# Kernel optimization log

Hardware: AMD Instinct MI355X
Metric: run time of the kernel (lower is better)

Reference implementation:

```python
import jax, jax.numpy as jnp
import numpy as np

EMBED_DIM = 1024
NUM_HEADS = 16
HEAD_DIM = EMBED_DIM // NUM_HEADS
B, T = 2, 2048


def setup_inputs() -> dict:
    key = jax.random.key(0)
    ks = jax.random.split(key, 9)
    s = 1.0 / np.sqrt(EMBED_DIM)
    return {
        "x": jax.random.normal(ks[0], (B, T, EMBED_DIM), dtype=jnp.float32),
        "W_q": jax.random.uniform(ks[1], (EMBED_DIM, EMBED_DIM), jnp.float32, -s, s),
        "b_q": jax.random.uniform(ks[2], (EMBED_DIM,), jnp.float32, -s, s),
        "W_k": jax.random.uniform(ks[3], (EMBED_DIM, EMBED_DIM), jnp.float32, -s, s),
        "b_k": jax.random.uniform(ks[4], (EMBED_DIM,), jnp.float32, -s, s),
        "W_v": jax.random.uniform(ks[5], (EMBED_DIM, EMBED_DIM), jnp.float32, -s, s),
        "b_v": jax.random.uniform(ks[6], (EMBED_DIM,), jnp.float32, -s, s),
        "W_o": jax.random.uniform(ks[7], (EMBED_DIM, EMBED_DIM), jnp.float32, -s, s),
        "b_o": jax.random.uniform(ks[8], (EMBED_DIM,), jnp.float32, -s, s),
    }


def reference(x, W_q, b_q, W_k, b_k, W_v, b_v, W_o, b_o):
    Bv, Tv, C = x.shape
    # QKV projections (torch Linear: x @ W.T + b); split into heads -> (B,H,T,Dh)
    def proj(W, b):
        return (x @ W.T + b).reshape(Bv, Tv, NUM_HEADS, HEAD_DIM).transpose(0, 2, 1, 3)
    q, k, v = proj(W_q, b_q), proj(W_k, b_k), proj(W_v, b_v)
    scale = 1.0 / np.sqrt(HEAD_DIM).astype(np.float32)
    scores = jnp.einsum("bhqd,bhkd->bhqk", q, k) * scale  # (B,H,T,T)
    causal = jnp.tril(jnp.ones((Tv, Tv), dtype=bool))
    scores = jnp.where(causal, scores, -jnp.inf)
    attn = jax.nn.softmax(scores, axis=-1)
    # dropout is identity in eval / p=0
    out = jnp.einsum("bhqk,bhkd->bhqd", attn, v)  # (B,H,T,Dh)
    out = out.transpose(0, 2, 1, 3).reshape(Bv, Tv, C)
    return out @ W_o.T + b_o
```

## Files before the change

### kernel.cpp

```cpp
#include <hip/hip_runtime.h>
#include <hip/hip_bf16.h>


typedef __bf16 bf16;
typedef __attribute__((ext_vector_type(8))) __bf16 bf16x8;
typedef __attribute__((ext_vector_type(4))) __bf16 bf16x4;
typedef __attribute__((ext_vector_type(4))) float floatx4;
typedef __attribute__((ext_vector_type(4))) short short4v;

#define LOG2E 1.44269504088896340736f

__device__ __forceinline__ void gl2lds16(const void* g, void* l) {
  __builtin_amdgcn_global_load_lds((const __attribute__((address_space(1))) void*)g,
                                   (__attribute__((address_space(3))) void*)l, 16, 0, 0);
}

__device__ __forceinline__ floatx4 mfma16(bf16x4 a, bf16x4 b, floatx4 c) {
#if __has_builtin(__builtin_amdgcn_mfma_f32_16x16x16_bf16)
  return __builtin_amdgcn_mfma_f32_16x16x16_bf16(a, b, c, 0, 0, 0);
#elif __has_builtin(__builtin_amdgcn_mfma_f32_16x16x16bf16_1k)
  return __builtin_amdgcn_mfma_f32_16x16x16bf16_1k(
      __builtin_bit_cast(short4v, a), __builtin_bit_cast(short4v, b), c, 0, 0, 0);
#else
  floatx4 d = c;
  asm volatile("v_mfma_f32_16x16x16_bf16 %0, %1, %2, %0"
               : "+v"(d) : "v"(a), "v"(b));
  return d;
#endif
}

__global__ __launch_bounds__(256) void cast_all(
    const float* __restrict__ x, const float* __restrict__ wq,
    const float* __restrict__ wk, const float* __restrict__ wv,
    const float* __restrict__ wo, bf16* __restrict__ dst)
{
  const size_t M1 = (size_t)1 << 20;
  size_t i4 = ((size_t)blockIdx.x * 256 + threadIdx.x) * 4;
  const float* src = x;
  size_t off = i4;
  if (i4 >= 4 * M1) {
    size_t r = i4 - 4 * M1;
    int seg = (int)(r >> 20);
    off = r & (M1 - 1);
    src = (seg == 0) ? wq : (seg == 1) ? wk : (seg == 2) ? wv : wo;
  }
  float4 f = *(const float4*)(src + off);
  bf16x4 o = { (bf16)f.x, (bf16)f.y, (bf16)f.z, (bf16)f.w };
  *(bf16x4*)(dst + i4) = o;
}

__global__ __launch_bounds__(256, 2) void gemm_qkv(
    const bf16* __restrict__ A, const bf16* __restrict__ Wb,
    const float* __restrict__ bq, const float* __restrict__ bk,
    const float* __restrict__ bv, bf16* __restrict__ Qout,
    bf16* __restrict__ Kout, bf16* __restrict__ vt, float qscale)
{
  constexpr int K = 1024;
  __shared__ bf16 As[128 * 64];
  __shared__ bf16 Bs[3][64 * 64];
  const int tid = threadIdx.x;
  const int lane = tid & 63;
  const int wid = tid >> 6;
  const int l15 = lane & 15, l4 = lane >> 4;
  const int n0 = blockIdx.x << 6;
  const int m0 = blockIdx.y << 7;

  floatx4 acc[3][2][4] = {};

  for (int k0 = 0; k0 < K; k0 += 64) {
#pragma unroll
    for (int it = 0; it < 4; ++it) {
      int c = it * 256 + tid;
      int row = c >> 3, gs = ((c & 7) ^ (row & 7)) << 3;
      gl2lds16(A + (size_t)(m0 + row) * K + k0 + gs, As + c * 8);
    }
#pragma unroll
    for (int mat = 0; mat < 3; ++mat)
#pragma unroll
      for (int it = 0; it < 2; ++it) {
        int c = it * 256 + tid;
        int row = c >> 3, gs = ((c & 7) ^ (row & 7)) << 3;
        gl2lds16(Wb + ((size_t)mat << 20) + (size_t)(n0 + row) * K + k0 + gs,
                 &Bs[mat][c * 8]);
      }
    __syncthreads();
#pragma unroll
    for (int kk = 0; kk < 2; ++kk) {
      bf16x8 af[2];
#pragma unroll
      for (int i = 0; i < 2; ++i) {
        int r = wid * 32 + i * 16 + l15;
        int g = (kk * 4 + l4) ^ (r & 7);
        af[i] = *(const bf16x8*)(As + r * 64 + g * 8);
      }
#pragma unroll
      for (int mat = 0; mat < 3; ++mat) {
        bf16x8 bfr[4];
#pragma unroll
        for (int j = 0; j < 4; ++j) {
          int r = j * 16 + l15;
          int g = (kk * 4 + l4) ^ (r & 7);
          bfr[j] = *(const bf16x8*)(&Bs[mat][r * 64 + g * 8]);
        }
#pragma unroll
        for (int i = 0; i < 2; ++i)
#pragma unroll
          for (int j = 0; j < 4; ++j)
            acc[mat][i][j] = __builtin_amdgcn_mfma_f32_16x16x32_bf16(
                af[i], bfr[j], acc[mat][i][j], 0, 0, 0);
      }
    }
    __syncthreads();
  }

#pragma unroll
  for (int j = 0; j < 4; ++j) {
    int col = n0 + j * 16 + l15;
    float bq_ = bq[col], bk_ = bk[col], bv_ = bv[col];
    int h = col >> 6, d = col & 63;
#pragma unroll
    for (int i = 0; i < 2; ++i) {
      int rbase = m0 + wid * 32 + i * 16 + l4 * 4;
#pragma unroll
      for (int rg = 0; rg < 4; ++rg) {
        int row = rbase + rg;
        Qout[(size_t)row * 1024 + col] = (bf16)((acc[0][i][j][rg] + bq_) * qscale);
        Kout[(size_t)row * 1024 + col] = (bf16)(acc[1][i][j][rg] + bk_);
      }
      int bb = rbase >> 11, t = rbase & 2047;
      int tp = (t & ~31) | (((t >> 2) & 3) << 3) | (((t >> 4) & 1) << 2);
      bf16x4 pk;
#pragma unroll
      for (int rg = 0; rg < 4; ++rg) pk[rg] = (bf16)(acc[2][i][j][rg] + bv_);
      *(bf16x4*)(vt + (((size_t)(bb * 16 + h)) << 17) + ((size_t)d << 11) + tp) = pk;
    }
  }
}

__global__ __launch_bounds__(256, 3) void gemm_out(
    const bf16* __restrict__ A, const bf16* __restrict__ W,
    const float* __restrict__ bias, float* __restrict__ outf, int K, int N)
{
  __shared__ bf16 As[128 * 64];
  __shared__ bf16 Bs[64 * 64];
  const int tid = threadIdx.x;
  const int lane = tid & 63;
  const int wid = tid >> 6;
  const int l15 = lane & 15, l4 = lane >> 4;
  const int n0 = blockIdx.x << 6;
  const int m0 = blockIdx.y << 7;

  floatx4 acc[2][4] = {};

  for (int k0 = 0; k0 < K; k0 += 64) {
#pragma unroll
    for (int it = 0; it < 4; ++it) {
      int c = it * 256 + tid;
      int row = c >> 3, gs = ((c & 7) ^ (row & 7)) << 3;
      gl2lds16(A + (size_t)(m0 + row) * K + k0 + gs, As + c * 8);
    }
#pragma unroll
    for (int it = 0; it < 2; ++it) {
      int c = it * 256 + tid;
      int row = c >> 3, gs = ((c & 7) ^ (row & 7)) << 3;
      gl2lds16(W + (size_t)(n0 + row) * K + k0 + gs, Bs + c * 8);
    }
    __syncthreads();
#pragma unroll
    for (int kk = 0; kk < 2; ++kk) {
      bf16x8 af[2], bfr[4];
#pragma unroll
      for (int i = 0; i < 2; ++i) {
        int r = wid * 32 + i * 16 + l15;
        int g = (kk * 4 + l4) ^ (r & 7);
        af[i] = *(const bf16x8*)(As + r * 64 + g * 8);
      }
#pragma unroll
      for (int j = 0; j < 4; ++j) {
        int r = j * 16 + l15;
        int g = (kk * 4 + l4) ^ (r & 7);
        bfr[j] = *(const bf16x8*)(Bs + r * 64 + g * 8);
      }
#pragma unroll
      for (int i = 0; i < 2; ++i)
#pragma unroll
        for (int j = 0; j < 4; ++j)
          acc[i][j] = __builtin_amdgcn_mfma_f32_16x16x32_bf16(af[i], bfr[j], acc[i][j], 0, 0, 0);
    }
    __syncthreads();
  }

#pragma unroll
  for (int j = 0; j < 4; ++j) {
    int col = n0 + j * 16 + l15;
    float b_ = bias[col];
#pragma unroll
    for (int i = 0; i < 2; ++i)
#pragma unroll
      for (int rg = 0; rg < 4; ++rg) {
        int row = m0 + wid * 32 + i * 16 + l4 * 4 + rg;
        outf[(size_t)row * N + col] = acc[i][j][rg] + b_;
      }
  }
}

__global__ __launch_bounds__(256, 3) void attn_kernel(
    const bf16* __restrict__ Q, const bf16* __restrict__ Kg,
    const bf16* __restrict__ Vt, bf16* __restrict__ AO)
{
  constexpr int T = 2048, C = 1024;
  __shared__ bf16 Ks[2][64 * 64];
  __shared__ bf16 Vts[2][64 * 64];

  const int tid = threadIdx.x;
  const int lane = tid & 63;
  const int w = tid >> 6;
  const int l15 = lane & 15, l4 = lane >> 4;

  const int u = blockIdx.x;
  const int bh = u & 31;
  const int qt = 31 - (u >> 5);
  const int q0 = qt << 6;
  const int nkt = qt + 1;
  const size_t base = ((size_t)(bh >> 4) * T) * C + (bh & 15) * 64;
  const bf16* vtb = Vt + ((size_t)bh << 17);

  auto stageK = [&](int j0, int bufi) {
#pragma unroll
    for (int it = 0; it < 2; ++it) {
      int c = it * 256 + tid;
      int row = c >> 3, g = (c & 7) ^ (row & 7);
      gl2lds16(Kg + base + (size_t)(j0 + row) * C + g * 8, &Ks[bufi][c * 8]);
    }
  };
  auto stageV = [&](int j0, int bufi) {
#pragma unroll
    for (int it = 0; it < 2; ++it) {
      int c = it * 256 + tid;
      int d = c >> 3, g = (c & 7) ^ (d & 7);
      gl2lds16(vtb + ((size_t)d << 11) + j0 + g * 8, &Vts[bufi][c * 8]);
    }
  };

  const int q = q0 + w * 16 + l15;

  bf16x8 qf[2];
  {
    const bf16* qp = Q + base + (size_t)q * C + l4 * 8;
    qf[0] = *(const bf16x8*)(qp);
    qf[1] = *(const bf16x8*)(qp + 32);
  }

  floatx4 o[4] = {};
  float lpart = 0.f;

  stageK(0, 0);
  stageV(0, 0);

  for (int jt = 0; jt < nkt; ++jt) {
    __syncthreads();
    const int cur = jt & 1;
    if (jt + 1 < nkt) {
      stageK((jt + 1) << 6, cur ^ 1);
      stageV((jt + 1) << 6, cur ^ 1);
    }
    const int j0 = jt << 6;

    floatx4 s4[4] = {};
#pragma unroll
    for (int kk = 0; kk < 2; ++kk) {
#pragma unroll
      for (int tj = 0; tj < 4; ++tj) {
        int r = tj * 16 + l15;
        int g = (kk * 4 + l4) ^ (r & 7);
        bf16x8 kf = *(const bf16x8*)(&Ks[cur][r * 64 + g * 8]);
        s4[tj] = __builtin_amdgcn_mfma_f32_16x16x32_bf16(kf, qf[kk], s4[tj], 0, 0, 0);
      }
    }

    if (jt == nkt - 1) {
#pragma unroll
      for (int tj = 0; tj < 4; ++tj) {
        int j = j0 + tj * 16 + l4 * 4;
#pragma unroll
        for (int rg = 0; rg < 4; ++rg)
          if (j + rg > q) s4[tj][rg] = -3e38f;
      }
    }

#pragma unroll
    for (int tj = 0; tj < 4; ++tj)
#pragma unroll
      for (int rg = 0; rg < 4; ++rg) {
        float e = __builtin_amdgcn_exp2f(s4[tj][rg]);
        s4[tj][rg] = e;
        lpart += e;
      }

    bf16x4 pf[4];
#pragma unroll
    for (int tj = 0; tj < 4; ++tj) {
      bf16x4 pk = { (bf16)s4[tj][0], (bf16)s4[tj][1],
                    (bf16)s4[tj][2], (bf16)s4[tj][3] };
      pf[tj] = pk;
    }

#pragma unroll
    for (int tk = 0; tk < 2; ++tk) {
#pragma unroll
      for (int td = 0; td < 4; ++td) {
        int r = td * 16 + l15;
        int g = (tk * 4 + l4) ^ (r & 7);
        bf16x8 vf = *(const bf16x8*)(&Vts[cur][r * 64 + g * 8]);
        bf16x4 lo = { vf[0], vf[1], vf[2], vf[3] };
        bf16x4 hi = { vf[4], vf[5], vf[6], vf[7] };
        o[td] = mfma16(lo, pf[tk * 2], o[td]);
        o[td] = mfma16(hi, pf[tk * 2 + 1], o[td]);
      }
    }
  }

  lpart += __shfl_xor(lpart, 16, 64);
  lpart += __shfl_xor(lpart, 32, 64);
  float inv = 1.0f / lpart;
#pragma unroll
  for (int td = 0; td < 4; ++td) {
    bf16x4 ok = { (bf16)(o[td][0] * inv), (bf16)(o[td][1] * inv),
                  (bf16)(o[td][2] * inv), (bf16)(o[td][3] * inv) };
    *(bf16x4*)(AO + base + (size_t)q * C + td * 16 + l4 * 4) = ok;
  }
}

extern "C" void kernel_launch(void* const* d_in, const int* in_sizes, int n_in,
                              void* d_out, int out_size, void* d_ws, size_t ws_size,
                              hipStream_t stream) {
  const float* x  = (const float*)d_in[0];
  const float* Wq = (const float*)d_in[1];
  const float* bq = (const float*)d_in[2];
  const float* Wk = (const float*)d_in[3];
  const float* bk = (const float*)d_in[4];
  const float* Wv = (const float*)d_in[5];
  const float* bv = (const float*)d_in[6];
  const float* Wo = (const float*)d_in[7];
  const float* bo = (const float*)d_in[8];

  bf16* ws = (bf16*)d_ws;
  const size_t M1 = (size_t)1 << 20;
  bf16* xb  = ws;
  bf16* wqb = ws + 4 * M1;
  bf16* wob = ws + 7 * M1;
  bf16* Qp  = ws + 8 * M1;
  bf16* Kp  = ws + 12 * M1;
  bf16* Vtp = ws + 16 * M1;
  bf16* AOp = ws + 20 * M1;

  cast_all<<<8192, 256, 0, stream>>>(x, Wq, Wk, Wv, Wo, ws);
  gemm_qkv<<<dim3(16, 32), 256, 0, stream>>>(
      xb, wqb, bq, bk, bv, Qp, Kp, Vtp, 0.125f * LOG2E);
  attn_kernel<<<1024, 256, 0, stream>>>(Qp, Kp, Vtp, AOp);
  gemm_out<<<dim3(16, 32), 256, 0, stream>>>(
      AOp, wob, bo, (float*)d_out, 1024, 1024);
}
```

Measured before the change: 169.1 us.

## Restructure QKV GEMM into 256x192 double-buffered tiles with interleaved loads and MFMAs

Rewrites the fused QKV projection GEMM to use 512-thread blocks covering 256x192 output tiles, treating the Q/K/V weights as one concatenated 3072-wide matrix. LDS is double-buffered, and the next tile's global-to-LDS loads are interleaved with MFMA phases using raw s_barrier and s_setprio, in a ping-pong style schedule. A block-index swizzle remaps the 1D grid onto tiles for cache locality. This is meant to hide memory latency and raise operand reuse per block, at the cost of more LDS and registers per block and fewer blocks overall (256).

```diff
diff --git a/kernel.cpp b/kernel.cpp
--- a/kernel.cpp
+++ b/kernel.cpp
@@ -28,6 +28,9 @@
   return d;
 #endif
 }
+
+#define MFMA32 __builtin_amdgcn_mfma_f32_16x16x32_bf16
+#define PBAR asm volatile("s_barrier" ::: "memory")
 
 __global__ __launch_bounds__(256) void cast_all(
     const float* __restrict__ x, const float* __restrict__ wq,
@@ -49,90 +52,164 @@
   *(bf16x4*)(dst + i4) = o;
 }
 
-__global__ __launch_bounds__(256, 2) void gemm_qkv(
+__global__ __launch_bounds__(512, 2) void gemm_qkv(
     const bf16* __restrict__ A, const bf16* __restrict__ Wb,
     const float* __restrict__ bq, const float* __restrict__ bk,
     const float* __restrict__ bv, bf16* __restrict__ Qout,
     bf16* __restrict__ Kout, bf16* __restrict__ vt, float qscale)
 {
   constexpr int K = 1024;
-  __shared__ bf16 As[128 * 64];
-  __shared__ bf16 Bs[3][64 * 64];
+  constexpr int NT = 16;
+  __shared__ bf16 As[2][256 * 64];
+  __shared__ bf16 Bs[2][192 * 64];
+
   const int tid = threadIdx.x;
   const int lane = tid & 63;
   const int wid = tid >> 6;
+  const int wm = wid >> 2;
+  const int wn = wid & 3;
   const int l15 = lane & 15, l4 = lane >> 4;
-  const int n0 = blockIdx.x << 6;
-  const int m0 = blockIdx.y << 7;
-
-  floatx4 acc[3][2][4] = {};
-
-  for (int k0 = 0; k0 < K; k0 += 64) {
+  const int xlo = l15 & 7;
+
+  const int u = blockIdx.x;
+  const int xk = u & 7, s = u >> 3;
+  const int by = xk * 2 + (s & 1);
+  const int bx = s >> 1;
+  const int m0 = by << 8;
+  const int n0 = bx * 192;
+
+  auto stageA = [&](int t) {
+    const int bufi = t & 1;
 #pragma unroll
     for (int it = 0; it < 4; ++it) {
-      int c = it * 256 + tid;
+      int c = it * 512 + tid;
       int row = c >> 3, gs = ((c & 7) ^ (row & 7)) << 3;
-      gl2lds16(A + (size_t)(m0 + row) * K + k0 + gs, As + c * 8);
-    }
-#pragma unroll
-    for (int mat = 0; mat < 3; ++mat)
-#pragma unroll
-      for (int it = 0; it < 2; ++it) {
-        int c = it * 256 + tid;
-        int row = c >> 3, gs = ((c & 7) ^ (row & 7)) << 3;
-        gl2lds16(Wb + ((size_t)mat << 20) + (size_t)(n0 + row) * K + k0 + gs,
-                 &Bs[mat][c * 8]);
-      }
+      gl2lds16(A + (size_t)(m0 + row) * K + t * 64 + gs, &As[bufi][c * 8]);
+    }
+  };
+  auto stageB = [&](int t) {
+    const int bufi = t & 1;
+#pragma unroll
+    for (int it = 0; it < 2; ++it) {
+      int c = it * 512 + tid;
+      int row = c >> 3, gs = ((c & 7) ^ (row & 7)) << 3;
+      gl2lds16(Wb + (size_t)(n0 + row) * K + t * 64 + gs, &Bs[bufi][c * 8]);
+    }
+    {
+      int c = 1024 + tid;
+      int row = c >> 3, gs = ((c & 7) ^ (row & 7)) << 3;
+      gl2lds16(Wb + (size_t)(n0 + row) * K + t * 64 + gs, &Bs[bufi][c * 8]);
+    }
+  };
+
+  floatx4 acc[8][3] = {};
+  bf16x8 a_[4][2];
+  bf16x8 b_[3][2];
+
+  stageA(0);
+  stageB(0);
+  __syncthreads();
+
+  for (int t = 0; t < NT; ++t) {
+    const int cur = t & 1;
+
+#pragma unroll
+    for (int f = 0; f < 4; ++f)
+#pragma unroll
+      for (int kk = 0; kk < 2; ++kk)
+        a_[f][kk] = *(const bf16x8*)(
+            &As[cur][(wm * 128 + f * 16 + l15) * 64 + (((kk * 4 + l4) ^ xlo) << 3)]);
+#pragma unroll
+    for (int j = 0; j < 2; ++j)
+#pragma unroll
+      for (int kk = 0; kk < 2; ++kk)
+        b_[j][kk] = *(const bf16x8*)(
+            &Bs[cur][(wn * 48 + j * 16 + l15) * 64 + (((kk * 4 + l4) ^ xlo) << 3)]);
+    if (t + 1 < NT) stageA(t + 1);
+    PBAR;
+    __builtin_amdgcn_s_setprio(1);
+#pragma unroll
+    for (int f = 0; f < 4; ++f)
+#pragma unroll
+      for (int j = 0; j < 2; ++j)
+#pragma unroll
+        for (int kk = 0; kk < 2; ++kk)
+          acc[f][j] = MFMA32(a_[f][kk], b_[j][kk], acc[f][j], 0, 0, 0);
+    __builtin_amdgcn_s_setprio(0);
+    PBAR;
+
+#pragma unroll
+    for (int kk = 0; kk < 2; ++kk)
+      b_[2][kk] = *(const bf16x8*)(
+          &Bs[cur][(wn * 48 + 32 + l15) * 64 + (((kk * 4 + l4) ^ xlo) << 3)]);
+    if (t + 1 < NT) stageB(t + 1);
+    PBAR;
+    __builtin_amdgcn_s_setprio(1);
+#pragma unroll
+    for (int f = 0; f < 4; ++f)
+#pragma unroll
+      for (int kk = 0; kk < 2; ++kk)
+        acc[f][2] = MFMA32(a_[f][kk], b_[2][kk], acc[f][2], 0, 0, 0);
+    __builtin_amdgcn_s_setprio(0);
+    PBAR;
+
+#pragma unroll
+    for (int f = 0; f < 4; ++f)
+#pragma unroll
+      for (int kk = 0; kk < 2; ++kk)
+        a_[f][kk] = *(const bf16x8*)(
+            &As[cur][(wm * 128 + 64 + f * 16 + l15) * 64 + (((kk * 4 + l4) ^ xlo) << 3)]);
+    PBAR;
+    __builtin_amdgcn_s_setprio(1);
+#pragma unroll
+    for (int f = 0; f < 4; ++f)
+#pragma unroll
+      for (int kk = 0; kk < 2; ++kk)
+        acc[4 + f][2] = MFMA32(a_[f][kk], b_[2][kk], acc[4 + f][2], 0, 0, 0);
+    __builtin_amdgcn_s_setprio(0);
+    PBAR;
+
+    __builtin_amdgcn_s_setprio(1);
+#pragma unroll
+    for (int f = 0; f < 4; ++f)
+#pragma unroll
+      for (int j = 0; j < 2; ++j)
+#pragma unroll
+        for (int kk = 0; kk < 2; ++kk)
+          acc[4 + f][j] = MFMA32(a_[f][kk], b_[j][kk], acc[4 + f][j], 0, 0, 0);
+    __builtin_amdgcn_s_setprio(0);
+
     __syncthreads();
-#pragma unroll
-    for (int kk = 0; kk < 2; ++kk) {
-      bf16x8 af[2];
-#pragma unroll
-      for (int i = 0; i < 2; ++i) {
-        int r = wid * 32 + i * 16 + l15;
-        int g = (kk * 4 + l4) ^ (r & 7);
-        af[i] = *(const bf16x8*)(As + r * 64 + g * 8);
-      }
-#pragma unroll
-      for (int mat = 0; mat < 3; ++mat) {
-        bf16x8 bfr[4];
-#pragma unroll
-        for (int j = 0; j < 4; ++j) {
-          int r = j * 16 + l15;
-          int g = (kk * 4 + l4) ^ (r & 7);
-          bfr[j] = *(const bf16x8*)(&Bs[mat][r * 64 + g * 8]);
-        }
-#pragma unroll
-        for (int i = 0; i < 2; ++i)
-#pragma unroll
-          for (int j = 0; j < 4; ++j)
-            acc[mat][i][j] = __builtin_amdgcn_mfma_f32_16x16x32_bf16(
-                af[i], bfr[j], acc[mat][i][j], 0, 0, 0);
-      }
-    }
-    __syncthreads();
-  }
-
-#pragma unroll
-  for (int j = 0; j < 4; ++j) {
-    int col = n0 + j * 16 + l15;
-    float bq_ = bq[col], bk_ = bk[col], bv_ = bv[col];
-    int h = col >> 6, d = col & 63;
-#pragma unroll
-    for (int i = 0; i < 2; ++i) {
-      int rbase = m0 + wid * 32 + i * 16 + l4 * 4;
-#pragma unroll
-      for (int rg = 0; rg < 4; ++rg) {
-        int row = rbase + rg;
-        Qout[(size_t)row * 1024 + col] = (bf16)((acc[0][i][j][rg] + bq_) * qscale);
-        Kout[(size_t)row * 1024 + col] = (bf16)(acc[1][i][j][rg] + bk_);
-      }
-      int bb = rbase >> 11, t = rbase & 2047;
-      int tp = (t & ~31) | (((t >> 2) & 3) << 3) | (((t >> 4) & 1) << 2);
-      bf16x4 pk;
-#pragma unroll
-      for (int rg = 0; rg < 4; ++rg) pk[rg] = (bf16)(acc[2][i][j][rg] + bv_);
-      *(bf16x4*)(vt + (((size_t)(bb * 16 + h)) << 17) + ((size_t)d << 11) + tp) = pk;
+  }
+
+#pragma unroll
+  for (int f = 0; f < 8; ++f) {
+    int rbase = m0 + wm * 128 + f * 16 + l4 * 4;
+#pragma unroll
+    for (int j = 0; j < 3; ++j) {
+      int col = n0 + wn * 48 + j * 16 + l15;
+      int mat = col >> 10;
+      int c10 = col & 1023;
+      floatx4 v = acc[f][j];
+      if (mat == 0) {
+        float b_ = bq[c10];
+#pragma unroll
+        for (int rg = 0; rg < 4; ++rg)
+          Qout[(size_t)(rbase + rg) * 1024 + c10] = (bf16)((v[rg] + b_) * qscale);
+      } else if (mat == 1) {
+        float b_ = bk[c10];
+#pragma unroll
+        for (int rg = 0; rg < 4; ++rg)
+          Kout[(size_t)(rbase + rg) * 1024 + c10] = (bf16)(v[rg] + b_);
+      } else {
+        float b_ = bv[c10];
+        int h = c10 >> 6, d = c10 & 63;
+        int bb = rbase >> 11, tt = rbase & 2047;
+        int tp = (tt & ~31) | (((tt >> 2) & 3) << 3) | (((tt >> 4) & 1) << 2);
+        bf16x4 pk = { (bf16)(v[0] + b_), (bf16)(v[1] + b_),
+                      (bf16)(v[2] + b_), (bf16)(v[3] + b_) };
+        *(bf16x4*)(vt + (((size_t)(bb * 16 + h)) << 17) + ((size_t)d << 11) + tp) = pk;
+      }
     }
   }
 }
@@ -185,7 +262,7 @@
       for (int i = 0; i < 2; ++i)
 #pragma unroll
         for (int j = 0; j < 4; ++j)
-          acc[i][j] = __builtin_amdgcn_mfma_f32_16x16x32_bf16(af[i], bfr[j], acc[i][j], 0, 0, 0);
+          acc[i][j] = MFMA32(af[i], bfr[j], acc[i][j], 0, 0, 0);
     }
     __syncthreads();
   }
@@ -355,7 +432,7 @@
   bf16* AOp = ws + 20 * M1;
 
   cast_all<<<8192, 256, 0, stream>>>(x, Wq, Wk, Wv, Wo, ws);
-  gemm_qkv<<<dim3(16, 32), 256, 0, stream>>>(
+  gemm_qkv<<<dim3(256), 512, 0, stream>>>(
       xb, wqb, bq, bk, bv, Qp, Kp, Vtp, 0.125f * LOG2E);
   attn_kernel<<<1024, 256, 0, stream>>>(Qp, Kp, Vtp, AOp);
   gemm_out<<<dim3(16, 32), 256, 0, stream>>>(
```

After: 173.6 us. 2.6% more time.

## Process two query tiles per attention block to reuse K/V tiles

Applied to the files above, without the earlier changes.

The attention kernel now has each block handle 128 query rows, split into two 64-row halves per wave, instead of 64. Each K/V tile staged in shared memory then feeds twice as many MFMAs, halving K/V global traffic and staging per query. Block scheduling is reordered to interleave long and short causal tiles for load balance. In exchange the grid shrinks to 512 blocks, register pressure rises (launch bounds relaxed from 3 to 2 blocks per CU), and the diagonal masking now spans two K tiles.

```diff
diff --git a/kernel.cpp b/kernel.cpp
--- a/kernel.cpp
+++ b/kernel.cpp
@@ -28,6 +28,8 @@
   return d;
 #endif
 }
+
+#define MFMA32 __builtin_amdgcn_mfma_f32_16x16x32_bf16
 
 __global__ __launch_bounds__(256) void cast_all(
     const float* __restrict__ x, const float* __restrict__ wq,
@@ -106,8 +108,7 @@
         for (int i = 0; i < 2; ++i)
 #pragma unroll
           for (int j = 0; j < 4; ++j)
-            acc[mat][i][j] = __builtin_amdgcn_mfma_f32_16x16x32_bf16(
-                af[i], bfr[j], acc[mat][i][j], 0, 0, 0);
+            acc[mat][i][j] = MFMA32(af[i], bfr[j], acc[mat][i][j], 0, 0, 0);
       }
     }
     __syncthreads();
@@ -185,7 +186,7 @@
       for (int i = 0; i < 2; ++i)
 #pragma unroll
         for (int j = 0; j < 4; ++j)
-          acc[i][j] = __builtin_amdgcn_mfma_f32_16x16x32_bf16(af[i], bfr[j], acc[i][j], 0, 0, 0);
+          acc[i][j] = MFMA32(af[i], bfr[j], acc[i][j], 0, 0, 0);
     }
     __syncthreads();
   }
@@ -204,7 +205,7 @@
   }
 }
 
-__global__ __launch_bounds__(256, 3) void attn_kernel(
+__global__ __launch_bounds__(256, 2) void attn_kernel(
     const bf16* __restrict__ Q, const bf16* __restrict__ Kg,
     const bf16* __restrict__ Vt, bf16* __restrict__ AO)
 {
@@ -219,9 +220,10 @@
 
   const int u = blockIdx.x;
   const int bh = u & 31;
-  const int qt = 31 - (u >> 5);
-  const int q0 = qt << 6;
-  const int nkt = qt + 1;
+  const int s = u >> 5;
+  const int qt = (s < 8) ? (15 - s) : (s - 8);
+  const int q0 = qt << 7;
+  const int nkt = (qt + 1) << 1;
   const size_t base = ((size_t)(bh >> 4) * T) * C + (bh & 15) * 64;
   const bf16* vtb = Vt + ((size_t)bh << 17);
 
@@ -242,17 +244,21 @@
     }
   };
 
-  const int q = q0 + w * 16 + l15;
-
-  bf16x8 qf[2];
+  const int qa = q0 + w * 16 + l15;
+  const int qb = qa + 64;
+
+  bf16x8 qf[2][2];
   {
-    const bf16* qp = Q + base + (size_t)q * C + l4 * 8;
-    qf[0] = *(const bf16x8*)(qp);
-    qf[1] = *(const bf16x8*)(qp + 32);
-  }
-
-  floatx4 o[4] = {};
-  float lpart = 0.f;
+    const bf16* qp = Q + base + (size_t)qa * C + l4 * 8;
+    qf[0][0] = *(const bf16x8*)(qp);
+    qf[0][1] = *(const bf16x8*)(qp + 32);
+    const bf16* qp1 = Q + base + (size_t)qb * C + l4 * 8;
+    qf[1][0] = *(const bf16x8*)(qp1);
+    qf[1][1] = *(const bf16x8*)(qp1 + 32);
+  }
+
+  floatx4 o[2][4] = {};
+  float lp0 = 0.f, lp1 = 0.f;
 
   stageK(0, 0);
   stageV(0, 0);
@@ -266,7 +272,7 @@
     }
     const int j0 = jt << 6;
 
-    floatx4 s4[4] = {};
+    floatx4 s4[2][4] = {};
 #pragma unroll
     for (int kk = 0; kk < 2; ++kk) {
 #pragma unroll
@@ -274,36 +280,35 @@
         int r = tj * 16 + l15;
         int g = (kk * 4 + l4) ^ (r & 7);
         bf16x8 kf = *(const bf16x8*)(&Ks[cur][r * 64 + g * 8]);
-        s4[tj] = __builtin_amdgcn_mfma_f32_16x16x32_bf16(kf, qf[kk], s4[tj], 0, 0, 0);
-      }
-    }
-
-    if (jt == nkt - 1) {
+        s4[0][tj] = MFMA32(kf, qf[0][kk], s4[0][tj], 0, 0, 0);
+        s4[1][tj] = MFMA32(kf, qf[1][kk], s4[1][tj], 0, 0, 0);
+      }
+    }
+
+    if (jt >= nkt - 2) {
 #pragma unroll
       for (int tj = 0; tj < 4; ++tj) {
         int j = j0 + tj * 16 + l4 * 4;
 #pragma unroll
-        for (int rg = 0; rg < 4; ++rg)
-          if (j + rg > q) s4[tj][rg] = -3e38f;
-      }
-    }
-
+        for (int rg = 0; rg < 4; ++rg) {
+          if (j + rg > qa) s4[0][tj][rg] = -3e38f;
+          if (j + rg > qb) s4[1][tj][rg] = -3e38f;
+        }
+      }
+    }
+
+    bf16x4 pf[2][4];
 #pragma unroll
     for (int tj = 0; tj < 4; ++tj)
 #pragma unroll
       for (int rg = 0; rg < 4; ++rg) {
-        float e = __builtin_amdgcn_exp2f(s4[tj][rg]);
-        s4[tj][rg] = e;
-        lpart += e;
-      }
-
-    bf16x4 pf[4];
-#pragma unroll
-    for (int tj = 0; tj < 4; ++tj) {
-      bf16x4 pk = { (bf16)s4[tj][0], (bf16)s4[tj][1],
-                    (bf16)s4[tj][2], (bf16)s4[tj][3] };
-      pf[tj] = pk;
-    }
+        float e0 = __builtin_amdgcn_exp2f(s4[0][tj][rg]);
+        float e1 = __builtin_amdgcn_exp2f(s4[1][tj][rg]);
+        lp0 += e0;
+        lp1 += e1;
+        pf[0][tj][rg] = (bf16)e0;
+        pf[1][tj][rg] = (bf16)e1;
+      }
 
 #pragma unroll
     for (int tk = 0; tk < 2; ++tk) {
@@ -314,20 +319,28 @@
         bf16x8 vf = *(const bf16x8*)(&Vts[cur][r * 64 + g * 8]);
         bf16x4 lo = { vf[0], vf[1], vf[2], vf[3] };
         bf16x4 hi = { vf[4], vf[5], vf[6], vf[7] };
-        o[td] = mfma16(lo, pf[tk * 2], o[td]);
-        o[td] = mfma16(hi, pf[tk * 2 + 1], o[td]);
-      }
-    }
-  }
-
-  lpart += __shfl_xor(lpart, 16, 64);
-  lpart += __shfl_xor(lpart, 32, 64);
-  float inv = 1.0f / lpart;
+        o[0][td] = mfma16(lo, pf[0][tk * 2], o[0][td]);
+        o[0][td] = mfma16(hi, pf[0][tk * 2 + 1], o[0][td]);
+        o[1][td] = mfma16(lo, pf[1][tk * 2], o[1][td]);
+        o[1][td] = mfma16(hi, pf[1][tk * 2 + 1], o[1][td]);
+      }
+    }
+  }
+
+  lp0 += __shfl_xor(lp0, 16, 64);
+  lp0 += __shfl_xor(lp0, 32, 64);
+  lp1 += __shfl_xor(lp1, 16, 64);
+  lp1 += __shfl_xor(lp1, 32, 64);
+  float inv0 = 1.0f / lp0;
+  float inv1 = 1.0f / lp1;
 #pragma unroll
   for (int td = 0; td < 4; ++td) {
-    bf16x4 ok = { (bf16)(o[td][0] * inv), (bf16)(o[td][1] * inv),
-                  (bf16)(o[td][2] * inv), (bf16)(o[td][3] * inv) };
-    *(bf16x4*)(AO + base + (size_t)q * C + td * 16 + l4 * 4) = ok;
+    bf16x4 ok0 = { (bf16)(o[0][td][0] * inv0), (bf16)(o[0][td][1] * inv0),
+                   (bf16)(o[0][td][2] * inv0), (bf16)(o[0][td][3] * inv0) };
+    *(bf16x4*)(AO + base + (size_t)qa * C + td * 16 + l4 * 4) = ok0;
+    bf16x4 ok1 = { (bf16)(o[1][td][0] * inv1), (bf16)(o[1][td][1] * inv1),
+                   (bf16)(o[1][td][2] * inv1), (bf16)(o[1][td][3] * inv1) };
+    *(bf16x4*)(AO + base + (size_t)qb * C + td * 16 + l4 * 4) = ok1;
   }
 }
 
@@ -357,7 +370,7 @@
   cast_all<<<8192, 256, 0, stream>>>(x, Wq, Wk, Wv, Wo, ws);
   gemm_qkv<<<dim3(16, 32), 256, 0, stream>>>(
       xb, wqb, bq, bk, bv, Qp, Kp, Vtp, 0.125f * LOG2E);
-  attn_kernel<<<1024, 256, 0, stream>>>(Qp, Kp, Vtp, AOp);
+  attn_kernel<<<512, 256, 0, stream>>>(Qp, Kp, Vtp, AOp);
   gemm_out<<<dim3(16, 32), 256, 0, stream>>>(
       AOp, wob, bo, (float*)d_out, 1024, 1024);
 }
```

New measurement: 176.2 us. 1.04x slower.

## Retile QKV and output GEMMs to 128x128 warp tiles with XCD-aware block mapping

Applied to the files above, without the earlier changes.

The QKV GEMM stops computing three 64-wide slices of Wq/Wk/Wv per block. It now treats the concatenated weights as one N=3072 matrix with 128x128 tiles, a 2x2 warp layout of 64x64 per warp, and a block-index swizzle that groups M tiles per XCD for L2 reuse. The epilogue branches on which matrix the tile belongs to. The output GEMM is likewise widened to 128x128 tiles, which halves its grid to 256 blocks. This raises arithmetic intensity per LDS load, but the smaller grid may underfill the 256 CUs, and register pressure rises under the higher occupancy bound.

```diff
diff --git a/kernel.cpp b/kernel.cpp
--- a/kernel.cpp
+++ b/kernel.cpp
@@ -28,6 +28,8 @@
   return d;
 #endif
 }
+
+#define MFMA32 __builtin_amdgcn_mfma_f32_16x16x32_bf16
 
 __global__ __launch_bounds__(256) void cast_all(
     const float* __restrict__ x, const float* __restrict__ wq,
@@ -49,7 +51,7 @@
   *(bf16x4*)(dst + i4) = o;
 }
 
-__global__ __launch_bounds__(256, 2) void gemm_qkv(
+__global__ __launch_bounds__(256, 3) void gemm_qkv(
     const bf16* __restrict__ A, const bf16* __restrict__ Wb,
     const float* __restrict__ bq, const float* __restrict__ bk,
     const float* __restrict__ bv, bf16* __restrict__ Qout,
@@ -57,15 +59,21 @@
 {
   constexpr int K = 1024;
   __shared__ bf16 As[128 * 64];
-  __shared__ bf16 Bs[3][64 * 64];
+  __shared__ bf16 Bs[128 * 64];
   const int tid = threadIdx.x;
   const int lane = tid & 63;
   const int wid = tid >> 6;
+  const int wm = wid >> 1, wn = wid & 1;
   const int l15 = lane & 15, l4 = lane >> 4;
-  const int n0 = blockIdx.x << 6;
-  const int m0 = blockIdx.y << 7;
-
-  floatx4 acc[3][2][4] = {};
+
+  const int u = blockIdx.x;
+  const int xcd = u & 7, s = u >> 3;
+  const int by = xcd * 4 + (s & 3);
+  const int bx = s >> 2;
+  const int m0 = by << 7;
+  const int n0 = bx << 7;
+
+  floatx4 acc[4][4] = {};
 
   for (int k0 = 0; k0 < K; k0 += 64) {
 #pragma unroll
@@ -75,64 +83,72 @@
       gl2lds16(A + (size_t)(m0 + row) * K + k0 + gs, As + c * 8);
     }
 #pragma unroll
-    for (int mat = 0; mat < 3; ++mat)
-#pragma unroll
-      for (int it = 0; it < 2; ++it) {
-        int c = it * 256 + tid;
-        int row = c >> 3, gs = ((c & 7) ^ (row & 7)) << 3;
-        gl2lds16(Wb + ((size_t)mat << 20) + (size_t)(n0 + row) * K + k0 + gs,
-                 &Bs[mat][c * 8]);
-      }
+    for (int it = 0; it < 4; ++it) {
+      int c = it * 256 + tid;
+      int row = c >> 3, gs = ((c & 7) ^ (row & 7)) << 3;
+      gl2lds16(Wb + (size_t)(n0 + row) * K + k0 + gs, Bs + c * 8);
+    }
     __syncthreads();
 #pragma unroll
     for (int kk = 0; kk < 2; ++kk) {
-      bf16x8 af[2];
-#pragma unroll
-      for (int i = 0; i < 2; ++i) {
-        int r = wid * 32 + i * 16 + l15;
+      bf16x8 af[4], bfr[4];
+#pragma unroll
+      for (int i = 0; i < 4; ++i) {
+        int r = wm * 64 + i * 16 + l15;
         int g = (kk * 4 + l4) ^ (r & 7);
         af[i] = *(const bf16x8*)(As + r * 64 + g * 8);
       }
 #pragma unroll
-      for (int mat = 0; mat < 3; ++mat) {
-        bf16x8 bfr[4];
-#pragma unroll
-        for (int j = 0; j < 4; ++j) {
-          int r = j * 16 + l15;
-          int g = (kk * 4 + l4) ^ (r & 7);
-          bfr[j] = *(const bf16x8*)(&Bs[mat][r * 64 + g * 8]);
-        }
-#pragma unroll
-        for (int i = 0; i < 2; ++i)
-#pragma unroll
-          for (int j = 0; j < 4; ++j)
-            acc[mat][i][j] = __builtin_amdgcn_mfma_f32_16x16x32_bf16(
-                af[i], bfr[j], acc[mat][i][j], 0, 0, 0);
-      }
-    }
-    __syncthreads();
-  }
-
+      for (int j = 0; j < 4; ++j) {
+        int r = wn * 64 + j * 16 + l15;
+        int g = (kk * 4 + l4) ^ (r & 7);
+        bfr[j] = *(const bf16x8*)(Bs + r * 64 + g * 8);
+      }
+#pragma unroll
+      for (int i = 0; i < 4; ++i)
+#pragma unroll
+        for (int j = 0; j < 4; ++j)
+          acc[i][j] = MFMA32(af[i], bfr[j], acc[i][j], 0, 0, 0);
+    }
+    __syncthreads();
+  }
+
+  const int mat = n0 >> 10;
 #pragma unroll
   for (int j = 0; j < 4; ++j) {
-    int col = n0 + j * 16 + l15;
-    float bq_ = bq[col], bk_ = bk[col], bv_ = bv[col];
-    int h = col >> 6, d = col & 63;
-#pragma unroll
-    for (int i = 0; i < 2; ++i) {
-      int rbase = m0 + wid * 32 + i * 16 + l4 * 4;
-#pragma unroll
-      for (int rg = 0; rg < 4; ++rg) {
-        int row = rbase + rg;
-        Qout[(size_t)row * 1024 + col] = (bf16)((acc[0][i][j][rg] + bq_) * qscale);
-        Kout[(size_t)row * 1024 + col] = (bf16)(acc[1][i][j][rg] + bk_);
-      }
-      int bb = rbase >> 11, t = rbase & 2047;
-      int tp = (t & ~31) | (((t >> 2) & 3) << 3) | (((t >> 4) & 1) << 2);
-      bf16x4 pk;
-#pragma unroll
-      for (int rg = 0; rg < 4; ++rg) pk[rg] = (bf16)(acc[2][i][j][rg] + bv_);
-      *(bf16x4*)(vt + (((size_t)(bb * 16 + h)) << 17) + ((size_t)d << 11) + tp) = pk;
+    int c10 = (n0 & 1023) + wn * 64 + j * 16 + l15;
+    if (mat == 0) {
+      float b_ = bq[c10];
+#pragma unroll
+      for (int i = 0; i < 4; ++i) {
+        int rbase = m0 + wm * 64 + i * 16 + l4 * 4;
+#pragma unroll
+        for (int rg = 0; rg < 4; ++rg)
+          Qout[(size_t)(rbase + rg) * 1024 + c10] =
+              (bf16)((acc[i][j][rg] + b_) * qscale);
+      }
+    } else if (mat == 1) {
+      float b_ = bk[c10];
+#pragma unroll
+      for (int i = 0; i < 4; ++i) {
+        int rbase = m0 + wm * 64 + i * 16 + l4 * 4;
+#pragma unroll
+        for (int rg = 0; rg < 4; ++rg)
+          Kout[(size_t)(rbase + rg) * 1024 + c10] = (bf16)(acc[i][j][rg] + b_);
+      }
+    } else {
+      float b_ = bv[c10];
+      int h = c10 >> 6, d = c10 & 63;
+#pragma unroll
+      for (int i = 0; i < 4; ++i) {
+        int rbase = m0 + wm * 64 + i * 16 + l4 * 4;
+        int bb = rbase >> 11, t = rbase & 2047;
+        int tp = (t & ~31) | (((t >> 2) & 3) << 3) | (((t >> 4) & 1) << 2);
+        bf16x4 pk;
+#pragma unroll
+        for (int rg = 0; rg < 4; ++rg) pk[rg] = (bf16)(acc[i][j][rg] + b_);
+        *(bf16x4*)(vt + (((size_t)(bb * 16 + h)) << 17) + ((size_t)d << 11) + tp) = pk;
+      }
     }
   }
 }
@@ -142,15 +158,16 @@
     const float* __restrict__ bias, float* __restrict__ outf, int K, int N)
 {
   __shared__ bf16 As[128 * 64];
-  __shared__ bf16 Bs[64 * 64];
+  __shared__ bf16 Bs[128 * 64];
   const int tid = threadIdx.x;
   const int lane = tid & 63;
   const int wid = tid >> 6;
+  const int wm = wid >> 1, wn = wid & 1;
   const int l15 = lane & 15, l4 = lane >> 4;
-  const int n0 = blockIdx.x << 6;
+  const int n0 = blockIdx.x << 7;
   const int m0 = blockIdx.y << 7;
 
-  floatx4 acc[2][4] = {};
+  floatx4 acc[4][4] = {};
 
   for (int k0 = 0; k0 < K; k0 += 64) {
 #pragma unroll
@@ -160,7 +177,7 @@
       gl2lds16(A + (size_t)(m0 + row) * K + k0 + gs, As + c * 8);
     }
 #pragma unroll
-    for (int it = 0; it < 2; ++it) {
+    for (int it = 0; it < 4; ++it) {
       int c = it * 256 + tid;
       int row = c >> 3, gs = ((c & 7) ^ (row & 7)) << 3;
       gl2lds16(W + (size_t)(n0 + row) * K + k0 + gs, Bs + c * 8);
@@ -168,37 +185,37 @@
     __syncthreads();
 #pragma unroll
     for (int kk = 0; kk < 2; ++kk) {
-      bf16x8 af[2], bfr[4];
-#pragma unroll
-      for (int i = 0; i < 2; ++i) {
-        int r = wid * 32 + i * 16 + l15;
+      bf16x8 af[4], bfr[4];
+#pragma unroll
+      for (int i = 0; i < 4; ++i) {
+        int r = wm * 64 + i * 16 + l15;
         int g = (kk * 4 + l4) ^ (r & 7);
         af[i] = *(const bf16x8*)(As + r * 64 + g * 8);
       }
 #pragma unroll
       for (int j = 0; j < 4; ++j) {
-        int r = j * 16 + l15;
+        int r = wn * 64 + j * 16 + l15;
         int g = (kk * 4 + l4) ^ (r & 7);
         bfr[j] = *(const bf16x8*)(Bs + r * 64 + g * 8);
       }
 #pragma unroll
-      for (int i = 0; i < 2; ++i)
+      for (int i = 0; i < 4; ++i)
 #pragma unroll
         for (int j = 0; j < 4; ++j)
-          acc[i][j] = __builtin_amdgcn_mfma_f32_16x16x32_bf16(af[i], bfr[j], acc[i][j], 0, 0, 0);
+          acc[i][j] = MFMA32(af[i], bfr[j], acc[i][j], 0, 0, 0);
     }
     __syncthreads();
   }
 
 #pragma unroll
   for (int j = 0; j < 4; ++j) {
-    int col = n0 + j * 16 + l15;
+    int col = n0 + wn * 64 + j * 16 + l15;
     float b_ = bias[col];
 #pragma unroll
-    for (int i = 0; i < 2; ++i)
+    for (int i = 0; i < 4; ++i)
 #pragma unroll
       for (int rg = 0; rg < 4; ++rg) {
-        int row = m0 + wid * 32 + i * 16 + l4 * 4 + rg;
+        int row = m0 + wm * 64 + i * 16 + l4 * 4 + rg;
         outf[(size_t)row * N + col] = acc[i][j][rg] + b_;
       }
   }
@@ -274,7 +291,7 @@
         int r = tj * 16 + l15;
         int g = (kk * 4 + l4) ^ (r & 7);
         bf16x8 kf = *(const bf16x8*)(&Ks[cur][r * 64 + g * 8]);
-        s4[tj] = __builtin_amdgcn_mfma_f32_16x16x32_bf16(kf, qf[kk], s4[tj], 0, 0, 0);
+        s4[tj] = MFMA32(kf, qf[kk], s4[tj], 0, 0, 0);
       }
     }
 
@@ -355,9 +372,9 @@
   bf16* AOp = ws + 20 * M1;
 
   cast_all<<<8192, 256, 0, stream>>>(x, Wq, Wk, Wv, Wo, ws);
-  gemm_qkv<<<dim3(16, 32), 256, 0, stream>>>(
+  gemm_qkv<<<768, 256, 0, stream>>>(
       xb, wqb, bq, bk, bv, Qp, Kp, Vtp, 0.125f * LOG2E);
   attn_kernel<<<1024, 256, 0, stream>>>(Qp, Kp, Vtp, AOp);
-  gemm_out<<<dim3(16, 32), 256, 0, stream>>>(
+  gemm_out<<<dim3(8, 32), 256, 0, stream>>>(
       AOp, wob, bo, (float*)d_out, 1024, 1024);
 }
```

Result: slower. 175.9 us (+4.0%).
